# Kernel tuning notes

Measured on AMD Instinct MI355X. Metric: run time of the kernel, lower is better.

## Reference

```python
import jax, jax.numpy as jnp
import numpy as np

B, N, C, H, P, K = 32, 4096, 64, 256, 8, 2


def setup_inputs() -> dict:
    key = jax.random.key(0)
    k1, k2, k3, k4 = jax.random.split(key, 4)
    s1 = 1.0 / np.sqrt(C)
    s2 = 1.0 / np.sqrt(H)
    return {
        "u_t": jax.random.normal(k1, (B, N, C), dtype=jnp.float32),
        "W1": jax.random.normal(k2, (P, C, H), dtype=jnp.float32) * s1,
        "b1": jnp.zeros((P, H), dtype=jnp.float32),
        "W2": jax.random.normal(k3, (P, H, C), dtype=jnp.float32) * s2,
        "b2": jnp.zeros((P, C), dtype=jnp.float32),
        "Wr": jax.random.normal(k4, (C, P), dtype=jnp.float32) * s1,
        "br": jnp.zeros((P,), dtype=jnp.float32),
        "top_k": K,
    }


def reference(u_t, W1, b1, W2, b2, Wr, br, top_k):
    # u_state = u_t[..., :output_channels]; here C_in == output_channels
    u_state = u_t
    # Router: mean-pool over spatial points -> per-sample logits over primitives
    pooled = jnp.mean(u_state, axis=1)                     # (B, C)
    logits = pooled @ Wr + br                              # (B, P)
    topk_vals, topk_idx = jax.lax.top_k(logits, top_k)     # (B, K)
    w = jax.nn.softmax(topk_vals, axis=-1)                 # (B, K) combine weights
    # Sparse dispatch: gather only the selected experts' params per sample
    W1e = W1[topk_idx]                                     # (B, K, C, H)
    b1e = b1[topk_idx]                                     # (B, K, H)
    W2e = W2[topk_idx]                                     # (B, K, H, C)
    b2e = b2[topk_idx]                                     # (B, K, C)
    # Primitive operator: pointwise 2-layer GELU MLP (erf gelu, torch default)
    h1 = jax.nn.gelu(jnp.einsum('bnc,bkch->bknh', u_t, W1e) + b1e[:, :, None, :],
                     approximate=False)                    # (B, K, N, H)
    delta = jnp.einsum('bknh,bkhc->bknc', h1, W2e) + b2e[:, :, None, :]  # (B, K, N, C)
    # Weighted combine: delta_sum = sum_k w_k * delta_k
    delta_sum = jnp.einsum('bknc,bk->bnc', delta, w)       # (B, N, C)
    return u_state + delta_sum
```

## Files before the change

### kernel.cpp

```cpp
#include <hip/hip_runtime.h>
#include <hip/hip_bf16.h>
#include <math.h>

#define B_ 32
#define N_ 4096
#define C_ 64
#define H_ 256
#define P_ 8

typedef short bf16x8 __attribute__((ext_vector_type(8)));
typedef float f32x4 __attribute__((ext_vector_type(4)));

__device__ __forceinline__ unsigned short f2bf(float f) {
    union { float f; unsigned int u; } v; v.f = f;
    unsigned int r = v.u + 0x7FFFu + ((v.u >> 16) & 1u);
    return (unsigned short)(r >> 16);
}

__global__ void pool_kernel(const float* __restrict__ u, float* __restrict__ pooled) {
    int b = blockIdx.y, chunk = blockIdx.x;
    int tid = threadIdx.x, c = tid & 63, rg = tid >> 6;
    const float* base = u + ((size_t)b * N_ + (size_t)chunk * 128) * C_;
    float s = 0.f;
    #pragma unroll 4
    for (int i = 0; i < 32; ++i) s += base[(i * 4 + rg) * C_ + c];
    __shared__ float red[4][64];
    red[rg][c] = s;
    __syncthreads();
    if (tid < 64) {
        float t = red[0][tid] + red[1][tid] + red[2][tid] + red[3][tid];
        atomicAdd(&pooled[b * C_ + tid], t);
    }
}

__global__ void router_kernel(const float* __restrict__ pooled, const float* __restrict__ Wr,
                              const float* __restrict__ br, float4* __restrict__ route) {
    int b = threadIdx.x;
    if (b >= B_) return;
    float lg[P_];
    for (int p = 0; p < P_; ++p) {
        float s = br[p];
        for (int c = 0; c < C_; ++c) s += pooled[b * C_ + c] * (1.0f / N_) * Wr[c * P_ + p];
        lg[p] = s;
    }
    int i0 = 0;
    for (int p = 1; p < P_; ++p) if (lg[p] > lg[i0]) i0 = p;
    int i1 = (i0 == 0) ? 1 : 0;
    for (int p = 0; p < P_; ++p) if (p != i0 && lg[p] > lg[i1]) i1 = p;
    float e1 = expf(lg[i1] - lg[i0]);
    float w0 = 1.f / (1.f + e1), w1 = e1 / (1.f + e1);
    route[b] = make_float4(w0, w1, __int_as_float(i0), __int_as_float(i1));
}

__global__ void prep_kernel(const float* __restrict__ W1, const float* __restrict__ W2,
                            unsigned short* __restrict__ W1T, unsigned short* __restrict__ W2T) {
    int idx = blockIdx.x * 256 + threadIdx.x;
    int e = idx >> 14, rem = idx & 16383, h = rem >> 6, c = rem & 63;
    W1T[idx] = f2bf(W1[(e << 14) + c * H_ + h]);
    W2T[(e << 14) + c * H_ + h] = f2bf(W2[idx]);
}

__global__ __launch_bounds__(256, 2)
void moe_main(const float* __restrict__ u, const float* __restrict__ b1,
              const float* __restrict__ b2, const unsigned short* __restrict__ W1T,
              const unsigned short* __restrict__ W2T, const float4* __restrict__ route,
              float* __restrict__ out) {
    __shared__ float uF[64][68];
    __shared__ unsigned short uA[64][72];
    __shared__ unsigned short h1s[64][264];

    const int b = blockIdx.y;
    const int n0 = blockIdx.x * 64;
    const int tid = threadIdx.x;

    const float4* up = (const float4*)(u + ((size_t)b * N_ + n0) * C_);
    #pragma unroll
    for (int i = 0; i < 4; ++i) {
        int idx = tid + 256 * i;
        int row = idx >> 4, c4 = idx & 15;
        float4 v = up[idx];
        *(float4*)&uF[row][c4 * 4] = v;
        ushort4 hv = make_ushort4(f2bf(v.x), f2bf(v.y), f2bf(v.z), f2bf(v.w));
        *(ushort4*)&uA[row][c4 * 4] = hv;
    }

    float4 rd = route[b];
    float wk2[2] = { rd.x, rd.y };
    int eidx[2] = { __float_as_int(rd.z), __float_as_int(rd.w) };

    const int lane = tid & 63, w = tid >> 6;
    const int r = lane & 15, g = lane >> 4;

    __syncthreads();

    float accOut[4][4];
    #pragma unroll
    for (int rt = 0; rt < 4; ++rt)
        #pragma unroll
        for (int j = 0; j < 4; ++j) accOut[rt][j] = 0.f;

    for (int ke = 0; ke < 2; ++ke) {
        const int e = eidx[ke];
        const float wk = wk2[ke];
        const unsigned short* w1e = W1T + (e << 14);
        const unsigned short* w2e = W2T + (e << 14);

        f32x4 acc1[4][4];
        #pragma unroll
        for (int ct = 0; ct < 4; ++ct)
            #pragma unroll
            for (int rt = 0; rt < 4; ++rt)
                #pragma unroll
                for (int q = 0; q < 4; ++q) acc1[ct][rt][q] = 0.f;

        #pragma unroll
        for (int ks = 0; ks < 2; ++ks) {
            bf16x8 a[4];
            #pragma unroll
            for (int rt = 0; rt < 4; ++rt)
                a[rt] = *(const bf16x8*)&uA[rt * 16 + r][ks * 32 + g * 8];
            #pragma unroll
            for (int ct = 0; ct < 4; ++ct) {
                int col = w * 64 + ct * 16 + r;
                bf16x8 bf = *(const bf16x8*)(w1e + col * C_ + ks * 32 + g * 8);
                #pragma unroll
                for (int rt = 0; rt < 4; ++rt)
                    acc1[ct][rt] = __builtin_amdgcn_mfma_f32_16x16x32_bf16(a[rt], bf, acc1[ct][rt], 0, 0, 0);
            }
        }
        #pragma unroll
        for (int ct = 0; ct < 4; ++ct) {
            int col = w * 64 + ct * 16 + r;
            float bias = b1[e * H_ + col];
            #pragma unroll
            for (int rt = 0; rt < 4; ++rt) {
                #pragma unroll
                for (int j = 0; j < 4; ++j) {
                    float x = acc1[ct][rt][j] + bias;
                    float gl = 0.5f * x * (1.f + erff(x * 0.70710678118654752f));
                    h1s[rt * 16 + g * 4 + j][col] = f2bf(gl);
                }
            }
        }
        __syncthreads();

        f32x4 acc2[4];
        #pragma unroll
        for (int rt = 0; rt < 4; ++rt)
            #pragma unroll
            for (int q = 0; q < 4; ++q) acc2[rt][q] = 0.f;
        const int c = w * 16 + r;
        #pragma unroll
        for (int ks2 = 0; ks2 < 8; ++ks2) {
            bf16x8 bf2 = *(const bf16x8*)(w2e + c * H_ + ks2 * 32 + g * 8);
            #pragma unroll
            for (int rt = 0; rt < 4; ++rt) {
                bf16x8 a2 = *(const bf16x8*)&h1s[rt * 16 + r][ks2 * 32 + g * 8];
                acc2[rt] = __builtin_amdgcn_mfma_f32_16x16x32_bf16(a2, bf2, acc2[rt], 0, 0, 0);
            }
        }
        float b2v = b2[e * C_ + c];
        #pragma unroll
        for (int rt = 0; rt < 4; ++rt)
            #pragma unroll
            for (int j = 0; j < 4; ++j)
                accOut[rt][j] += wk * (acc2[rt][j] + b2v);
        __syncthreads();
    }

    const int cc = w * 16 + r;
    #pragma unroll
    for (int rt = 0; rt < 4; ++rt) {
        #pragma unroll
        for (int j = 0; j < 4; ++j) {
            int row = rt * 16 + g * 4 + j;
            out[((size_t)b * N_ + n0 + row) * C_ + cc] = uF[row][cc] + accOut[rt][j];
        }
    }
}

extern "C" void kernel_launch(void* const* d_in, const int* in_sizes, int n_in,
                              void* d_out, int out_size, void* d_ws, size_t ws_size,
                              hipStream_t stream) {
    const float* u  = (const float*)d_in[0];
    const float* W1 = (const float*)d_in[1];
    const float* b1 = (const float*)d_in[2];
    const float* W2 = (const float*)d_in[3];
    const float* b2 = (const float*)d_in[4];
    const float* Wr = (const float*)d_in[5];
    const float* br = (const float*)d_in[6];
    float* out = (float*)d_out;

    char* ws = (char*)d_ws;
    float* pooled = (float*)ws;
    float4* route = (float4*)(ws + 8192);
    unsigned short* W1T = (unsigned short*)(ws + 16384);
    unsigned short* W2T = (unsigned short*)(ws + 16384 + 262144);

    hipMemsetAsync(pooled, 0, 2048 * sizeof(float), stream);
    prep_kernel<<<512, 256, 0, stream>>>(W1, W2, W1T, W2T);
    pool_kernel<<<dim3(32, 32), 256, 0, stream>>>(u, pooled);
    router_kernel<<<1, 64, 0, stream>>>(pooled, Wr, br, route);
    moe_main<<<dim3(64, 32), 256, 0, stream>>>(u, b1, b2, W1T, W2T, route, out);
}
```

Measured before the change: 197.9 us.

## Fuse prep/pool and router into main kernel, tanh GELU, coalesced output

Merges the weight-transpose and pooling kernels into one launch and folds the router's top-2 and softmax into each main block, removing two launches. Replaces erf GELU with a tanh approximation using fast exp. Swaps MFMA operand roles so h1 is written as vector stores, and stages the output through shared memory for coalesced float4 writes that re-read u from global. Drops the fp32 u tile and raises launch bounds to 3 blocks per SM for occupancy. The tanh GELU changes numerics slightly.

After: 192.0 us. -3.0%, faster.

```diff
diff --git a/kernel.cpp b/kernel.cpp
--- a/kernel.cpp
+++ b/kernel.cpp
@@ -17,9 +17,29 @@
     return (unsigned short)(r >> 16);
 }
 
-__global__ void pool_kernel(const float* __restrict__ u, float* __restrict__ pooled) {
-    int b = blockIdx.y, chunk = blockIdx.x;
-    int tid = threadIdx.x, c = tid & 63, rg = tid >> 6;
+__device__ __forceinline__ float gelu_f(float x) {
+    float x2 = x * x;
+    float y = x * fmaf(0.044715f * 0.7978845608028654f, x2, 0.7978845608028654f);
+    float e = __expf(2.f * y);
+    float t = 1.f - 2.f / (e + 1.f);
+    return 0.5f * x * (1.f + t);
+}
+
+__global__ void prep_pool_kernel(const float* __restrict__ W1, const float* __restrict__ W2,
+                                 const float* __restrict__ u,
+                                 unsigned short* __restrict__ W1T, unsigned short* __restrict__ W2T,
+                                 float* __restrict__ pooled) {
+    int bid = blockIdx.x, tid = threadIdx.x;
+    if (bid < 512) {
+        int idx = bid * 256 + tid;
+        int e = idx >> 14, rem = idx & 16383, h = rem >> 6, c = rem & 63;
+        W1T[idx] = f2bf(W1[(e << 14) + c * H_ + h]);
+        W2T[(e << 14) + c * H_ + h] = f2bf(W2[idx]);
+        return;
+    }
+    int pb = bid - 512;
+    int b = pb >> 5, chunk = pb & 31;
+    int c = tid & 63, rg = tid >> 6;
     const float* base = u + ((size_t)b * N_ + (size_t)chunk * 128) * C_;
     float s = 0.f;
     #pragma unroll 4
@@ -33,65 +53,58 @@
     }
 }
 
-__global__ void router_kernel(const float* __restrict__ pooled, const float* __restrict__ Wr,
-                              const float* __restrict__ br, float4* __restrict__ route) {
-    int b = threadIdx.x;
-    if (b >= B_) return;
-    float lg[P_];
-    for (int p = 0; p < P_; ++p) {
-        float s = br[p];
-        for (int c = 0; c < C_; ++c) s += pooled[b * C_ + c] * (1.0f / N_) * Wr[c * P_ + p];
-        lg[p] = s;
-    }
-    int i0 = 0;
-    for (int p = 1; p < P_; ++p) if (lg[p] > lg[i0]) i0 = p;
-    int i1 = (i0 == 0) ? 1 : 0;
-    for (int p = 0; p < P_; ++p) if (p != i0 && lg[p] > lg[i1]) i1 = p;
-    float e1 = expf(lg[i1] - lg[i0]);
-    float w0 = 1.f / (1.f + e1), w1 = e1 / (1.f + e1);
-    route[b] = make_float4(w0, w1, __int_as_float(i0), __int_as_float(i1));
-}
-
-__global__ void prep_kernel(const float* __restrict__ W1, const float* __restrict__ W2,
-                            unsigned short* __restrict__ W1T, unsigned short* __restrict__ W2T) {
-    int idx = blockIdx.x * 256 + threadIdx.x;
-    int e = idx >> 14, rem = idx & 16383, h = rem >> 6, c = rem & 63;
-    W1T[idx] = f2bf(W1[(e << 14) + c * H_ + h]);
-    W2T[(e << 14) + c * H_ + h] = f2bf(W2[idx]);
-}
-
-__global__ __launch_bounds__(256, 2)
+__global__ __launch_bounds__(256, 3)
 void moe_main(const float* __restrict__ u, const float* __restrict__ b1,
               const float* __restrict__ b2, const unsigned short* __restrict__ W1T,
-              const unsigned short* __restrict__ W2T, const float4* __restrict__ route,
+              const unsigned short* __restrict__ W2T, const float* __restrict__ pooled,
+              const float* __restrict__ Wr, const float* __restrict__ br,
               float* __restrict__ out) {
-    __shared__ float uF[64][68];
-    __shared__ unsigned short uA[64][72];
-    __shared__ unsigned short h1s[64][264];
+    __shared__ __align__(16) unsigned short uA[64][72];
+    __shared__ __align__(16) unsigned short h1s[64][264];
+    __shared__ float lgS[8];
 
     const int b = blockIdx.y;
     const int n0 = blockIdx.x * 64;
     const int tid = threadIdx.x;
 
     const float4* up = (const float4*)(u + ((size_t)b * N_ + n0) * C_);
+    float4 v[4];
+    #pragma unroll
+    for (int i = 0; i < 4; ++i) v[i] = up[tid + 256 * i];
+
+    if (tid < 8) {
+        float s = br[tid];
+        const float* pb = pooled + b * C_;
+        #pragma unroll
+        for (int c = 0; c < C_; ++c) s += pb[c] * (1.0f / N_) * Wr[c * P_ + tid];
+        lgS[tid] = s;
+    }
+
     #pragma unroll
     for (int i = 0; i < 4; ++i) {
         int idx = tid + 256 * i;
         int row = idx >> 4, c4 = idx & 15;
-        float4 v = up[idx];
-        *(float4*)&uF[row][c4 * 4] = v;
-        ushort4 hv = make_ushort4(f2bf(v.x), f2bf(v.y), f2bf(v.z), f2bf(v.w));
+        ushort4 hv = make_ushort4(f2bf(v[i].x), f2bf(v[i].y), f2bf(v[i].z), f2bf(v[i].w));
         *(ushort4*)&uA[row][c4 * 4] = hv;
     }
-
-    float4 rd = route[b];
-    float wk2[2] = { rd.x, rd.y };
-    int eidx[2] = { __float_as_int(rd.z), __float_as_int(rd.w) };
+    __syncthreads();
+
+    float lg[8];
+    #pragma unroll
+    for (int p = 0; p < 8; ++p) lg[p] = lgS[p];
+    int i0 = 0;
+    #pragma unroll
+    for (int p = 1; p < 8; ++p) if (lg[p] > lg[i0]) i0 = p;
+    int i1 = (i0 == 0) ? 1 : 0;
+    #pragma unroll
+    for (int p = 0; p < 8; ++p) if (p != i0 && lg[p] > lg[i1]) i1 = p;
+    float e1 = __expf(lg[i1] - lg[i0]);
+    float w0r = 1.f / (1.f + e1);
+    float wk2[2] = { w0r, e1 * w0r };
+    int eidx[2] = { i0, i1 };
 
     const int lane = tid & 63, w = tid >> 6;
     const int r = lane & 15, g = lane >> 4;
-
-    __syncthreads();
 
     float accOut[4][4];
     #pragma unroll
@@ -115,31 +128,32 @@
 
         #pragma unroll
         for (int ks = 0; ks < 2; ++ks) {
-            bf16x8 a[4];
+            bf16x8 bu[4];
             #pragma unroll
             for (int rt = 0; rt < 4; ++rt)
-                a[rt] = *(const bf16x8*)&uA[rt * 16 + r][ks * 32 + g * 8];
+                bu[rt] = *(const bf16x8*)&uA[rt * 16 + r][ks * 32 + g * 8];
             #pragma unroll
             for (int ct = 0; ct < 4; ++ct) {
-                int col = w * 64 + ct * 16 + r;
-                bf16x8 bf = *(const bf16x8*)(w1e + col * C_ + ks * 32 + g * 8);
+                int hrow = w * 64 + ct * 16 + r;
+                bf16x8 aw = *(const bf16x8*)(w1e + hrow * C_ + ks * 32 + g * 8);
                 #pragma unroll
                 for (int rt = 0; rt < 4; ++rt)
-                    acc1[ct][rt] = __builtin_amdgcn_mfma_f32_16x16x32_bf16(a[rt], bf, acc1[ct][rt], 0, 0, 0);
+                    acc1[ct][rt] = __builtin_amdgcn_mfma_f32_16x16x32_bf16(aw, bu[rt], acc1[ct][rt], 0, 0, 0);
             }
         }
+
         #pragma unroll
         for (int ct = 0; ct < 4; ++ct) {
-            int col = w * 64 + ct * 16 + r;
-            float bias = b1[e * H_ + col];
+            int hbase = w * 64 + ct * 16 + g * 4;
+            float4 bias = *(const float4*)(b1 + e * H_ + hbase);
             #pragma unroll
             for (int rt = 0; rt < 4; ++rt) {
-                #pragma unroll
-                for (int j = 0; j < 4; ++j) {
-                    float x = acc1[ct][rt][j] + bias;
-                    float gl = 0.5f * x * (1.f + erff(x * 0.70710678118654752f));
-                    h1s[rt * 16 + g * 4 + j][col] = f2bf(gl);
-                }
+                float g0 = gelu_f(acc1[ct][rt][0] + bias.x);
+                float g1 = gelu_f(acc1[ct][rt][1] + bias.y);
+                float g2 = gelu_f(acc1[ct][rt][2] + bias.z);
+                float g3 = gelu_f(acc1[ct][rt][3] + bias.w);
+                ushort4 hv = make_ushort4(f2bf(g0), f2bf(g1), f2bf(g2), f2bf(g3));
+                *(ushort4*)&h1s[rt * 16 + r][hbase] = hv;
             }
         }
         __syncthreads();
@@ -152,11 +166,11 @@
         const int c = w * 16 + r;
         #pragma unroll
         for (int ks2 = 0; ks2 < 8; ++ks2) {
-            bf16x8 bf2 = *(const bf16x8*)(w2e + c * H_ + ks2 * 32 + g * 8);
+            bf16x8 bw = *(const bf16x8*)(w2e + c * H_ + ks2 * 32 + g * 8);
             #pragma unroll
             for (int rt = 0; rt < 4; ++rt) {
-                bf16x8 a2 = *(const bf16x8*)&h1s[rt * 16 + r][ks2 * 32 + g * 8];
-                acc2[rt] = __builtin_amdgcn_mfma_f32_16x16x32_bf16(a2, bf2, acc2[rt], 0, 0, 0);
+                bf16x8 ah = *(const bf16x8*)&h1s[rt * 16 + r][ks2 * 32 + g * 8];
+                acc2[rt] = __builtin_amdgcn_mfma_f32_16x16x32_bf16(ah, bw, acc2[rt], 0, 0, 0);
             }
         }
         float b2v = b2[e * C_ + c];
@@ -168,14 +182,24 @@
         __syncthreads();
     }
 
-    const int cc = w * 16 + r;
-    #pragma unroll
-    for (int rt = 0; rt < 4; ++rt) {
-        #pragma unroll
-        for (int j = 0; j < 4; ++j) {
-            int row = rt * 16 + g * 4 + j;
-            out[((size_t)b * N_ + n0 + row) * C_ + cc] = uF[row][cc] + accOut[rt][j];
-        }
+    float* dS = (float*)&h1s[0][0];
+    {
+        const int c = w * 16 + r;
+        #pragma unroll
+        for (int rt = 0; rt < 4; ++rt)
+            #pragma unroll
+            for (int j = 0; j < 4; ++j)
+                dS[(rt * 16 + g * 4 + j) * 68 + c] = accOut[rt][j];
+    }
+    __syncthreads();
+    float4* op = (float4*)(out + ((size_t)b * N_ + n0) * C_);
+    #pragma unroll
+    for (int i = 0; i < 4; ++i) {
+        int idx = tid + 256 * i;
+        int row = idx >> 4, c4 = idx & 15;
+        float4 uv = up[idx];
+        float4 dv = *(float4*)&dS[row * 68 + c4 * 4];
+        op[idx] = make_float4(uv.x + dv.x, uv.y + dv.y, uv.z + dv.z, uv.w + dv.w);
     }
 }
 
@@ -193,13 +217,10 @@
 
     char* ws = (char*)d_ws;
     float* pooled = (float*)ws;
-    float4* route = (float4*)(ws + 8192);
     unsigned short* W1T = (unsigned short*)(ws + 16384);
     unsigned short* W2T = (unsigned short*)(ws + 16384 + 262144);
 
     hipMemsetAsync(pooled, 0, 2048 * sizeof(float), stream);
-    prep_kernel<<<512, 256, 0, stream>>>(W1, W2, W1T, W2T);
-    pool_kernel<<<dim3(32, 32), 256, 0, stream>>>(u, pooled);
-    router_kernel<<<1, 64, 0, stream>>>(pooled, Wr, br, route);
-    moe_main<<<dim3(64, 32), 256, 0, stream>>>(u, b1, b2, W1T, W2T, route, out);
-}
+    prep_pool_kernel<<<1536, 256, 0, stream>>>(W1, W2, u, W1T, W2T, pooled);
+    moe_main<<<dim3(64, 32), 256, 0, stream>>>(u, b1, b2, W1T, W2T, pooled, Wr, br, out);
+}
```

## Fuse prep/pool/router into one kernel and keep MLP hidden layer in registers

Applied to the files above, without the earlier changes.

Merges weight conversion, mean pooling and routing into a single launch, using a last-block atomic counter to run the router. The main kernel now gives each wavefront its own 64-row slab and loads u straight into bf16 registers. The hidden layer is computed in chunks of 32 columns whose GELU output feeds the second MFMA directly, removing the shared-memory staging and barriers. To make this work, W1 and b1 are permuted so the first MFMA's output layout matches the A-operand layout of the second. It also folds the combine weight into a cheap exp2-based GELU approximation and sums the two experts' biases once at the end. The GELU approximation and bf16 b1 bias add accuracy risk, and u is re-read from global memory for the residual.

New measurement: 167.3 us. 1.18x faster.

```diff
diff --git a/kernel.cpp b/kernel.cpp
--- a/kernel.cpp
+++ b/kernel.cpp
@@ -7,176 +7,242 @@
 #define C_ 64
 #define H_ 256
 #define P_ 8
+#define NPOOL 1024
 
 typedef short bf16x8 __attribute__((ext_vector_type(8)));
 typedef float f32x4 __attribute__((ext_vector_type(4)));
+
+union BF8 { bf16x8 v; unsigned int w[4]; };
 
 __device__ __forceinline__ unsigned short f2bf(float f) {
     union { float f; unsigned int u; } v; v.f = f;
     unsigned int r = v.u + 0x7FFFu + ((v.u >> 16) & 1u);
     return (unsigned short)(r >> 16);
 }
-
-__global__ void pool_kernel(const float* __restrict__ u, float* __restrict__ pooled) {
-    int b = blockIdx.y, chunk = blockIdx.x;
-    int tid = threadIdx.x, c = tid & 63, rg = tid >> 6;
+__device__ __forceinline__ float bf2f(unsigned short h) {
+    union { float f; unsigned int u; } v; v.u = ((unsigned int)h) << 16; return v.f;
+}
+__device__ __forceinline__ unsigned int pk_bf16(float lo, float hi) {
+    unsigned int r;
+    asm("v_cvt_pk_bf16_f32 %0, %1, %2" : "=v"(r) : "v"(lo), "v"(hi));
+    return r;
+}
+__device__ __forceinline__ float gelu_w(float x, float wk) {
+    float x2 = x * x;
+    float y2 = x * fmaf(0.10294322f, x2, 2.30220772f);
+    float e  = __builtin_amdgcn_exp2f(y2);
+    float rc = __builtin_amdgcn_rcpf(e + 1.0f);
+    float wx = wk * x;
+    return fmaf(-wx, rc, wx);
+}
+
+__device__ __forceinline__ int hperm(int t, int d) {
+    return ((t >> 1) << 5) + ((d >> 2) << 3) + ((t & 1) << 2) + (d & 3);
+}
+
+__global__ void prep_pool(const float* __restrict__ W1, const float* __restrict__ W2,
+                          const float* __restrict__ b1, const float* __restrict__ u,
+                          const float* __restrict__ Wr, const float* __restrict__ br,
+                          unsigned short* __restrict__ W1P, unsigned short* __restrict__ W2T,
+                          unsigned short* __restrict__ b1P, float* __restrict__ pooled,
+                          int* __restrict__ counter, float4* __restrict__ route) {
+    int bid = blockIdx.x, tid = threadIdx.x;
+    if (bid < 512) {
+        int oi = bid * 256 + tid;
+        int e = oi >> 14, rowP = (oi >> 6) & 255, c = oi & 63;
+        int h = hperm(rowP >> 4, rowP & 15);
+        W1P[oi] = f2bf(W1[(e << 14) + (c << 8) + h]);
+        return;
+    }
+    if (bid < 1024) {
+        int oi = (bid - 512) * 256 + tid;
+        int e = oi >> 14, c = (oi >> 8) & 63, h = oi & 255;
+        W2T[oi] = f2bf(W2[(e << 14) + (h << 6) + c]);
+        return;
+    }
+    if (bid < 1032) {
+        int oi = (bid - 1024) * 256 + tid;
+        int e = oi >> 8, idx = oi & 255;
+        int h = hperm(idx >> 4, idx & 15);
+        b1P[oi] = f2bf(b1[(e << 8) + h]);
+        return;
+    }
+    int pb = bid - 1032;
+    int b = pb >> 5, chunk = pb & 31;
+    int c = tid & 63, rg = tid >> 6;
     const float* base = u + ((size_t)b * N_ + (size_t)chunk * 128) * C_;
     float s = 0.f;
     #pragma unroll 4
     for (int i = 0; i < 32; ++i) s += base[(i * 4 + rg) * C_ + c];
     __shared__ float red[4][64];
+    __shared__ int isLast;
+    __shared__ float lgAll[B_][P_];
     red[rg][c] = s;
     __syncthreads();
     if (tid < 64) {
-        float t = red[0][tid] + red[1][tid] + red[2][tid] + red[3][tid];
-        atomicAdd(&pooled[b * C_ + tid], t);
-    }
-}
-
-__global__ void router_kernel(const float* __restrict__ pooled, const float* __restrict__ Wr,
-                              const float* __restrict__ br, float4* __restrict__ route) {
-    int b = threadIdx.x;
-    if (b >= B_) return;
-    float lg[P_];
-    for (int p = 0; p < P_; ++p) {
-        float s = br[p];
-        for (int c = 0; c < C_; ++c) s += pooled[b * C_ + c] * (1.0f / N_) * Wr[c * P_ + p];
-        lg[p] = s;
-    }
-    int i0 = 0;
-    for (int p = 1; p < P_; ++p) if (lg[p] > lg[i0]) i0 = p;
-    int i1 = (i0 == 0) ? 1 : 0;
-    for (int p = 0; p < P_; ++p) if (p != i0 && lg[p] > lg[i1]) i1 = p;
-    float e1 = expf(lg[i1] - lg[i0]);
-    float w0 = 1.f / (1.f + e1), w1 = e1 / (1.f + e1);
-    route[b] = make_float4(w0, w1, __int_as_float(i0), __int_as_float(i1));
-}
-
-__global__ void prep_kernel(const float* __restrict__ W1, const float* __restrict__ W2,
-                            unsigned short* __restrict__ W1T, unsigned short* __restrict__ W2T) {
-    int idx = blockIdx.x * 256 + threadIdx.x;
-    int e = idx >> 14, rem = idx & 16383, h = rem >> 6, c = rem & 63;
-    W1T[idx] = f2bf(W1[(e << 14) + c * H_ + h]);
-    W2T[(e << 14) + c * H_ + h] = f2bf(W2[idx]);
+        float t4 = red[0][tid] + red[1][tid] + red[2][tid] + red[3][tid];
+        atomicAdd(&pooled[b * C_ + tid], t4);
+        __threadfence();
+    }
+    __syncthreads();
+    if (tid == 0) {
+        int old = atomicAdd(counter, 1);
+        isLast = (old == NPOOL - 1);
+    }
+    __syncthreads();
+    if (!isLast) return;
+    __threadfence();
+    {
+        int rb = tid >> 3, p = tid & 7;
+        const float* pb2 = pooled + rb * C_;
+        float sacc = br[p];
+        #pragma unroll
+        for (int cc = 0; cc < C_; ++cc) {
+            float pv = __hip_atomic_load(&pb2[cc], __ATOMIC_RELAXED, __HIP_MEMORY_SCOPE_AGENT);
+            sacc += pv * (1.0f / N_) * Wr[cc * P_ + p];
+        }
+        lgAll[rb][p] = sacc;
+    }
+    __syncthreads();
+    if (tid < B_) {
+        float lg[P_];
+        #pragma unroll
+        for (int p = 0; p < P_; ++p) lg[p] = lgAll[tid][p];
+        int i0 = 0;
+        #pragma unroll
+        for (int p = 1; p < P_; ++p) if (lg[p] > lg[i0]) i0 = p;
+        int i1 = (i0 == 0) ? 1 : 0;
+        #pragma unroll
+        for (int p = 0; p < P_; ++p) if (p != i0 && lg[p] > lg[i1]) i1 = p;
+        float e1 = __expf(lg[i1] - lg[i0]);
+        float w0 = 1.f / (1.f + e1);
+        route[tid] = make_float4(w0, e1 * w0, __int_as_float(i0), __int_as_float(i1));
+    }
 }
 
 __global__ __launch_bounds__(256, 2)
-void moe_main(const float* __restrict__ u, const float* __restrict__ b1,
-              const float* __restrict__ b2, const unsigned short* __restrict__ W1T,
-              const unsigned short* __restrict__ W2T, const float4* __restrict__ route,
+void moe_main(const float* __restrict__ u, const unsigned short* __restrict__ W1P,
+              const unsigned short* __restrict__ W2T, const unsigned short* __restrict__ b1P,
+              const float* __restrict__ b2, const float4* __restrict__ route,
               float* __restrict__ out) {
-    __shared__ float uF[64][68];
-    __shared__ unsigned short uA[64][72];
-    __shared__ unsigned short h1s[64][264];
-
-    const int b = blockIdx.y;
-    const int n0 = blockIdx.x * 64;
     const int tid = threadIdx.x;
-
-    const float4* up = (const float4*)(u + ((size_t)b * N_ + n0) * C_);
-    #pragma unroll
-    for (int i = 0; i < 4; ++i) {
-        int idx = tid + 256 * i;
-        int row = idx >> 4, c4 = idx & 15;
-        float4 v = up[idx];
-        *(float4*)&uF[row][c4 * 4] = v;
-        ushort4 hv = make_ushort4(f2bf(v.x), f2bf(v.y), f2bf(v.z), f2bf(v.w));
-        *(ushort4*)&uA[row][c4 * 4] = hv;
-    }
+    const int wv = tid >> 6, lane = tid & 63;
+    const int r = lane & 15, g = lane >> 4;
+    const int b = blockIdx.x >> 4;
+    const int nslab = ((blockIdx.x & 15) << 2) + wv;
+    const int n0 = nslab << 6;
 
     float4 rd = route[b];
-    float wk2[2] = { rd.x, rd.y };
-    int eidx[2] = { __float_as_int(rd.z), __float_as_int(rd.w) };
-
-    const int lane = tid & 63, w = tid >> 6;
-    const int r = lane & 15, g = lane >> 4;
-
-    __syncthreads();
-
-    float accOut[4][4];
-    #pragma unroll
-    for (int rt = 0; rt < 4; ++rt)
-        #pragma unroll
-        for (int j = 0; j < 4; ++j) accOut[rt][j] = 0.f;
+    const float wk2[2] = { rd.x, rd.y };
+    const int eidx[2] = { __float_as_int(rd.z), __float_as_int(rd.w) };
+
+    const float* ubase = u + ((size_t)b * N_ + n0) * C_;
+    bf16x8 ub[4][2];
+    #pragma unroll
+    for (int rt = 0; rt < 4; ++rt) {
+        const float* rp = ubase + (rt * 16 + r) * C_;
+        #pragma unroll
+        for (int ks = 0; ks < 2; ++ks) {
+            float4 lo = *(const float4*)(rp + ks * 32 + g * 8);
+            float4 hi = *(const float4*)(rp + ks * 32 + g * 8 + 4);
+            BF8 t;
+            t.w[0] = pk_bf16(lo.x, lo.y); t.w[1] = pk_bf16(lo.z, lo.w);
+            t.w[2] = pk_bf16(hi.x, hi.y); t.w[3] = pk_bf16(hi.z, hi.w);
+            ub[rt][ks] = t.v;
+        }
+    }
+
+    f32x4 acc2[4][4];
+    #pragma unroll
+    for (int ct = 0; ct < 4; ++ct)
+        #pragma unroll
+        for (int rt = 0; rt < 4; ++rt)
+            #pragma unroll
+            for (int q = 0; q < 4; ++q) acc2[ct][rt][q] = 0.f;
 
     for (int ke = 0; ke < 2; ++ke) {
         const int e = eidx[ke];
         const float wk = wk2[ke];
-        const unsigned short* w1e = W1T + (e << 14);
-        const unsigned short* w2e = W2T + (e << 14);
-
-        f32x4 acc1[4][4];
-        #pragma unroll
-        for (int ct = 0; ct < 4; ++ct)
-            #pragma unroll
-            for (int rt = 0; rt < 4; ++rt)
-                #pragma unroll
-                for (int q = 0; q < 4; ++q) acc1[ct][rt][q] = 0.f;
-
-        #pragma unroll
-        for (int ks = 0; ks < 2; ++ks) {
-            bf16x8 a[4];
-            #pragma unroll
-            for (int rt = 0; rt < 4; ++rt)
-                a[rt] = *(const bf16x8*)&uA[rt * 16 + r][ks * 32 + g * 8];
+        const unsigned short* w1p = W1P + (e << 14);
+        const unsigned short* w2t = W2T + (e << 14);
+        const unsigned short* b1e = b1P + (e << 8);
+
+        #pragma unroll
+        for (int tp = 0; tp < 8; ++tp) {
+            bf16x8 a1[2][2];
+            #pragma unroll
+            for (int tt = 0; tt < 2; ++tt)
+                #pragma unroll
+                for (int ks = 0; ks < 2; ++ks)
+                    a1[tt][ks] = *(const bf16x8*)(w1p + ((tp * 32 + tt * 16 + r) << 6) + ks * 32 + g * 8);
+            f32x4 acc1[2][4];
+            #pragma unroll
+            for (int tt = 0; tt < 2; ++tt)
+                #pragma unroll
+                for (int rt = 0; rt < 4; ++rt)
+                    #pragma unroll
+                    for (int q = 0; q < 4; ++q) acc1[tt][rt][q] = 0.f;
+            #pragma unroll
+            for (int ks = 0; ks < 2; ++ks)
+                #pragma unroll
+                for (int tt = 0; tt < 2; ++tt)
+                    #pragma unroll
+                    for (int rt = 0; rt < 4; ++rt)
+                        acc1[tt][rt] = __builtin_amdgcn_mfma_f32_16x16x32_bf16(
+                            a1[tt][ks], ub[rt][ks], acc1[tt][rt], 0, 0, 0);
+
+            float bv[8];
+            {
+                const unsigned short* bp = b1e + tp * 32 + 4 * g;
+                #pragma unroll
+                for (int j = 0; j < 4; ++j) { bv[j] = bf2f(bp[j]); bv[4 + j] = bf2f(bp[16 + j]); }
+            }
+            bf16x8 a2[4];
+            #pragma unroll
+            for (int rt = 0; rt < 4; ++rt) {
+                float gv[8];
+                #pragma unroll
+                for (int j = 0; j < 4; ++j) {
+                    gv[j]     = gelu_w(acc1[0][rt][j] + bv[j],     wk);
+                    gv[4 + j] = gelu_w(acc1[1][rt][j] + bv[4 + j], wk);
+                }
+                BF8 t;
+                t.w[0] = pk_bf16(gv[0], gv[1]); t.w[1] = pk_bf16(gv[2], gv[3]);
+                t.w[2] = pk_bf16(gv[4], gv[5]); t.w[3] = pk_bf16(gv[6], gv[7]);
+                a2[rt] = t.v;
+            }
+
+            bf16x8 b2f[4];
+            #pragma unroll
+            for (int ct = 0; ct < 4; ++ct)
+                b2f[ct] = *(const bf16x8*)(w2t + ((ct * 16 + r) << 8) + tp * 32 + g * 8);
+            #pragma unroll
+            for (int ct = 0; ct < 4; ++ct)
+                #pragma unroll
+                for (int rt = 0; rt < 4; ++rt)
+                    acc2[ct][rt] = __builtin_amdgcn_mfma_f32_16x16x32_bf16(
+                        a2[rt], b2f[ct], acc2[ct][rt], 0, 0, 0);
+        }
+    }
+
+    float bsum[4];
+    #pragma unroll
+    for (int ct = 0; ct < 4; ++ct) {
+        int c = ct * 16 + r;
+        bsum[ct] = wk2[0] * b2[eidx[0] * C_ + c] + wk2[1] * b2[eidx[1] * C_ + c];
+    }
+    float* obase = out + ((size_t)b * N_ + n0) * C_;
+    #pragma unroll
+    for (int rt = 0; rt < 4; ++rt)
+        #pragma unroll
+        for (int j = 0; j < 4; ++j) {
+            int row = rt * 16 + 4 * g + j;
             #pragma unroll
             for (int ct = 0; ct < 4; ++ct) {
-                int col = w * 64 + ct * 16 + r;
-                bf16x8 bf = *(const bf16x8*)(w1e + col * C_ + ks * 32 + g * 8);
-                #pragma unroll
-                for (int rt = 0; rt < 4; ++rt)
-                    acc1[ct][rt] = __builtin_amdgcn_mfma_f32_16x16x32_bf16(a[rt], bf, acc1[ct][rt], 0, 0, 0);
+                int c = ct * 16 + r;
+                obase[row * C_ + c] = ubase[row * C_ + c] + acc2[ct][rt][j] + bsum[ct];
             }
         }
-        #pragma unroll
-        for (int ct = 0; ct < 4; ++ct) {
-            int col = w * 64 + ct * 16 + r;
-            float bias = b1[e * H_ + col];
-            #pragma unroll
-            for (int rt = 0; rt < 4; ++rt) {
-                #pragma unroll
-                for (int j = 0; j < 4; ++j) {
-                    float x = acc1[ct][rt][j] + bias;
-                    float gl = 0.5f * x * (1.f + erff(x * 0.70710678118654752f));
-                    h1s[rt * 16 + g * 4 + j][col] = f2bf(gl);
-                }
-            }
-        }
-        __syncthreads();
-
-        f32x4 acc2[4];
-        #pragma unroll
-        for (int rt = 0; rt < 4; ++rt)
-            #pragma unroll
-            for (int q = 0; q < 4; ++q) acc2[rt][q] = 0.f;
-        const int c = w * 16 + r;
-        #pragma unroll
-        for (int ks2 = 0; ks2 < 8; ++ks2) {
-            bf16x8 bf2 = *(const bf16x8*)(w2e + c * H_ + ks2 * 32 + g * 8);
-            #pragma unroll
-            for (int rt = 0; rt < 4; ++rt) {
-                bf16x8 a2 = *(const bf16x8*)&h1s[rt * 16 + r][ks2 * 32 + g * 8];
-                acc2[rt] = __builtin_amdgcn_mfma_f32_16x16x32_bf16(a2, bf2, acc2[rt], 0, 0, 0);
-            }
-        }
-        float b2v = b2[e * C_ + c];
-        #pragma unroll
-        for (int rt = 0; rt < 4; ++rt)
-            #pragma unroll
-            for (int j = 0; j < 4; ++j)
-                accOut[rt][j] += wk * (acc2[rt][j] + b2v);
-        __syncthreads();
-    }
-
-    const int cc = w * 16 + r;
-    #pragma unroll
-    for (int rt = 0; rt < 4; ++rt) {
-        #pragma unroll
-        for (int j = 0; j < 4; ++j) {
-            int row = rt * 16 + g * 4 + j;
-            out[((size_t)b * N_ + n0 + row) * C_ + cc] = uF[row][cc] + accOut[rt][j];
-        }
-    }
 }
 
 extern "C" void kernel_launch(void* const* d_in, const int* in_sizes, int n_in,
@@ -192,14 +258,14 @@
     float* out = (float*)d_out;
 
     char* ws = (char*)d_ws;
-    float* pooled = (float*)ws;
-    float4* route = (float4*)(ws + 8192);
-    unsigned short* W1T = (unsigned short*)(ws + 16384);
-    unsigned short* W2T = (unsigned short*)(ws + 16384 + 262144);
-
-    hipMemsetAsync(pooled, 0, 2048 * sizeof(float), stream);
-    prep_kernel<<<512, 256, 0, stream>>>(W1, W2, W1T, W2T);
-    pool_kernel<<<dim3(32, 32), 256, 0, stream>>>(u, pooled);
-    router_kernel<<<1, 64, 0, stream>>>(pooled, Wr, br, route);
-    moe_main<<<dim3(64, 32), 256, 0, stream>>>(u, b1, b2, W1T, W2T, route, out);
-}
+    float* pooled        = (float*)ws;
+    int* counter         = (int*)(ws + 8192);
+    float4* route        = (float4*)(ws + 8256);
+    unsigned short* b1P  = (unsigned short*)(ws + 8768);
+    unsigned short* W1P  = (unsigned short*)(ws + 16384);
+    unsigned short* W2T  = (unsigned short*)(ws + 16384 + 262144);
+
+    hipMemsetAsync(ws, 0, 8256, stream);
+    prep_pool<<<2056, 256, 0, stream>>>(W1, W2, b1, u, Wr, br, W1P, W2T, b1P, pooled, counter, route);
+    moe_main<<<512, 256, 0, stream>>>(u, W1P, W2T, b1P, b2, route, out);
+}
```
